# Optimization experiments

Hardware: AMD Instinct MI355X
Metric: run time of the kernel (lower is better)

Reference implementation:

```python
import jax, jax.numpy as jnp
import numpy as np

DIM = 4096
N_HEADS = 32
HEAD_DIM = DIM // N_HEADS
BSZ = 4
SEQLEN = 512
MAX_SEQ = 2048
NEG = -1e9


def _qlinear(x, q, s):
    # int-quantized weight [out,in] dequantized with per-output-channel scale
    w = q.astype(jnp.float32) * s[:, None]
    return jnp.einsum('bsd,od->bso', x, w)


def _apply_rotary(xq, xk, cos, sin):
    # xq,xk: [b,s,h,hd]; cos,sin: [s,hd/2]
    def rot(t):
        b, s, h, d = t.shape
        t = t.reshape(b, s, h, d // 2, 2)
        tr, ti = t[..., 0], t[..., 1]
        c = cos[None, :, None, :]
        sn = sin[None, :, None, :]
        out_r = tr * c - ti * sn
        out_i = tr * sn + ti * c
        return jnp.stack([out_r, out_i], axis=-1).reshape(b, s, h, d)
    return rot(xq), rot(xk)


def setup_inputs() -> dict:
    key = jax.random.key(0)
    ks = jax.random.split(key, 12)
    x = jax.random.normal(ks[0], (BSZ, SEQLEN, DIM), dtype=jnp.float32)
    inv = 1.0 / (10000.0 ** (jnp.arange(0, HEAD_DIM, 2, dtype=jnp.float32) / HEAD_DIM))
    ang = jnp.arange(SEQLEN, dtype=jnp.float32)[:, None] * inv[None, :]
    freqs_cos, freqs_sin = jnp.cos(ang), jnp.sin(ang)
    input_idexes = jnp.arange(SEQLEN, dtype=jnp.int32)  # cache slots being written
    # causal additive mask over full cache: query at position i may attend j <= i
    j = jnp.arange(MAX_SEQ)
    mask = jnp.where(j[None, :] <= input_idexes[:, None], 0.0, NEG).astype(jnp.float32)
    mask = mask[None, None]  # [1,1,S,MAX_SEQ]
    cache_k = jnp.zeros((BSZ, MAX_SEQ, N_HEADS, HEAD_DIM), jnp.float32)
    cache_v = jnp.zeros((BSZ, MAX_SEQ, N_HEADS, HEAD_DIM), jnp.float32)
    SCALE = 2.0 / (127.0 * np.sqrt(DIM))
    def mkw(kq, kscale):
        q = jax.random.randint(kq, (DIM, DIM), -127, 128, dtype=jnp.int32)
        s = jax.random.uniform(kscale, (DIM,), dtype=jnp.float32) * SCALE
        return q, s
    wq_q, wq_s = mkw(ks[1], ks[2])
    wk_q, wk_s = mkw(ks[3], ks[4])
    wv_q, wv_s = mkw(ks[5], ks[6])
    wo_q, wo_s = mkw(ks[7], ks[8])
    return dict(x=x, freqs_cos=freqs_cos, freqs_sin=freqs_sin, mask=mask,
                input_idexes=input_idexes, cache_k=cache_k, cache_v=cache_v,
                wq_q=wq_q, wq_s=wq_s, wk_q=wk_q, wk_s=wk_s,
                wv_q=wv_q, wv_s=wv_s, wo_q=wo_q, wo_s=wo_s)


def reference(x, freqs_cos, freqs_sin, mask, input_idexes, cache_k, cache_v,
              wq_q, wq_s, wk_q, wk_s, wv_q, wv_s, wo_q, wo_s):
    bsz, seqlen, _ = x.shape
    xq = _qlinear(x, wq_q, wq_s).reshape(bsz, seqlen, N_HEADS, HEAD_DIM)
    xk = _qlinear(x, wk_q, wk_s).reshape(bsz, seqlen, N_HEADS, HEAD_DIM)
    xv = _qlinear(x, wv_q, wv_s).reshape(bsz, seqlen, N_HEADS, HEAD_DIM)
    xq, xk = _apply_rotary(xq, xk, freqs_cos, freqs_sin)
    # KV-cache append (index_copy on dim 1)
    cache_k = cache_k.at[:, input_idexes].set(xk)
    cache_v = cache_v.at[:, input_idexes].set(xv)
    # [b,h,q,d] x [b,h,k,d] -> [b,h,q,k]
    scores = jnp.einsum('bqhd,bkhd->bhqk', xq, cache_k) / np.sqrt(HEAD_DIM)
    scores = scores + mask
    probs = jax.nn.softmax(scores.astype(jnp.float32), axis=-1).astype(xq.dtype)
    out = jnp.einsum('bhqk,bkhd->bqhd', probs, cache_v).reshape(bsz, seqlen, -1)
    out = _qlinear(out, wo_q, wo_s)
    return out, (cache_k, cache_v)
```

## Files before the change

kernel.cpp:

```cpp
#include <hip/hip_runtime.h>
#include <cstdint>
#include <cstddef>

typedef __bf16 bf16;
typedef __attribute__((ext_vector_type(8))) __bf16 bf16x8;
typedef __attribute__((ext_vector_type(2))) __bf16 bf16x2;
typedef __attribute__((ext_vector_type(4))) float f32x4;
typedef __attribute__((ext_vector_type(2))) float f32x2;
typedef __attribute__((ext_vector_type(4))) int i32x4;

#define DIMN 4096
#define SEQ 512
#define MAXSEQ 2048
#define NHEAD 32
#define HD 128
#define NBH 128
#define MTOK 2048

#define BM 128
#define BN 128
#define BK 32
#define BKI 64

__device__ __forceinline__ void gld_lds16(const void* g, void* l) {
  __builtin_amdgcn_global_load_lds(
      (const __attribute__((address_space(1))) unsigned int*)g,
      (__attribute__((address_space(3))) unsigned int*)l, 16, 0, 0);
}

__device__ __forceinline__ void gemm_core(const bf16* Ablk, const bf16* Bblk,
                                          int lda, int ldb, int kmax,
                                          f32x4 acc[4][4], bf16* As, bf16* Bs) {
  const int tid = threadIdx.x;
  const int wave = tid >> 6;
  const int lane = tid & 63;
  const int wm = (wave >> 1) * 64;
  const int wn = (wave & 1) * 64;
  const int lrow = lane & 15;
  const int lkq8 = (lane >> 4) * 8;
  const int srow = wave * 32 + (lane >> 2);
  const int scol = (lane & 3) * 8;
  const bf16* Ag = Ablk + (size_t)srow * lda + scol;
  const bf16* Bg = Bblk + (size_t)srow * ldb + scol;
  bf16* lA = As + wave * 32 * BK;
  bf16* lB = Bs + wave * 32 * BK;

  for (int k0 = 0; k0 < kmax; k0 += BK) {
    __syncthreads();
    gld_lds16(Ag + k0, lA);
    gld_lds16(Ag + k0 + (size_t)16 * lda, lA + 16 * BK);
    gld_lds16(Bg + k0, lB);
    gld_lds16(Bg + k0 + (size_t)16 * ldb, lB + 16 * BK);
    __syncthreads();
    bf16x8 a[4], b[4];
#pragma unroll
    for (int i = 0; i < 4; ++i)
      a[i] = *(const bf16x8*)(As + (wm + i * 16 + lrow) * BK + lkq8);
#pragma unroll
    for (int i = 0; i < 4; ++i)
      b[i] = *(const bf16x8*)(Bs + (wn + i * 16 + lrow) * BK + lkq8);
#pragma unroll
    for (int mi = 0; mi < 4; ++mi)
#pragma unroll
      for (int ni = 0; ni < 4; ++ni)
        acc[mi][ni] = __builtin_amdgcn_mfma_f32_16x16x32_bf16(a[mi], b[ni], acc[mi][ni], 0, 0, 0);
  }
}

__device__ __forceinline__ void gemm_core_i8(const char* Ablk, const char* Bblk,
                                             int lda, int ldb, int kmax,
                                             i32x4 acc[4][4], char* As, char* Bs) {
  const int tid = threadIdx.x;
  const int wave = tid >> 6;
  const int lane = tid & 63;
  const int wm = (wave >> 1) * 64;
  const int wn = (wave & 1) * 64;
  const int lrow = lane & 15;
  const int lkq16 = (lane >> 4) * 16;
  const int srow = wave * 32 + (lane >> 2);
  const int scol = (lane & 3) * 16;
  const char* Ag = Ablk + (size_t)srow * lda + scol;
  const char* Bg = Bblk + (size_t)srow * ldb + scol;
  char* lA = As + wave * 32 * BKI;
  char* lB = Bs + wave * 32 * BKI;

  for (int k0 = 0; k0 < kmax; k0 += BKI) {
    __syncthreads();
    gld_lds16(Ag + k0, lA);
    gld_lds16(Ag + k0 + (size_t)16 * lda, lA + 16 * BKI);
    gld_lds16(Bg + k0, lB);
    gld_lds16(Bg + k0 + (size_t)16 * ldb, lB + 16 * BKI);
    __syncthreads();
    i32x4 a[4], b[4];
#pragma unroll
    for (int i = 0; i < 4; ++i)
      a[i] = *(const i32x4*)(As + (wm + i * 16 + lrow) * BKI + lkq16);
#pragma unroll
    for (int i = 0; i < 4; ++i)
      b[i] = *(const i32x4*)(Bs + (wn + i * 16 + lrow) * BKI + lkq16);
#pragma unroll
    for (int mi = 0; mi < 4; ++mi)
#pragma unroll
      for (int ni = 0; ni < 4; ++ni)
        acc[mi][ni] = __builtin_amdgcn_mfma_i32_16x16x64_i8(a[mi], b[ni], acc[mi][ni], 0, 0, 0);
  }
}

#define ACC_INIT_F(acc)                                 \
  f32x4 acc[4][4];                                      \
  _Pragma("unroll") for (int _i = 0; _i < 4; ++_i)      \
      _Pragma("unroll") for (int _j = 0; _j < 4; ++_j)  \
          acc[_i][_j] = f32x4{0.f, 0.f, 0.f, 0.f};

#define ACC_INIT_I(acc)                                 \
  i32x4 acc[4][4];                                      \
  _Pragma("unroll") for (int _i = 0; _i < 4; ++_i)      \
      _Pragma("unroll") for (int _j = 0; _j < 4; ++_j)  \
          acc[_i][_j] = i32x4{0, 0, 0, 0};

#define EPI_COORDS                                      \
  const int lane = threadIdx.x & 63;                    \
  const int wave = threadIdx.x >> 6;                    \
  const int wm = (wave >> 1) * 64, wn = (wave & 1) * 64;\
  const int cq = (lane >> 4) * 4, cc = lane & 15;

__global__ __launch_bounds__(256) void k_cvt_w8(
    const int* __restrict__ q0, const int* __restrict__ q1,
    const int* __restrict__ q2, const int* __restrict__ q3,
    char* __restrict__ w8) {
  const int* q = (blockIdx.y == 0) ? q0 : (blockIdx.y == 1) ? q1
               : (blockIdx.y == 2) ? q2 : q3;
  char* w = w8 + (size_t)blockIdx.y * 16777216ull;
  size_t i = ((size_t)blockIdx.x * 256 + threadIdx.x) * 16;
  const i32x4* qp = (const i32x4*)(q + i);
  i32x4 a = qp[0], b = qp[1], c = qp[2], d = qp[3];
  i32x4 o;
  o[0] = (a[0] & 255) | ((a[1] & 255) << 8) | ((a[2] & 255) << 16) | (a[3] << 24);
  o[1] = (b[0] & 255) | ((b[1] & 255) << 8) | ((b[2] & 255) << 16) | (b[3] << 24);
  o[2] = (c[0] & 255) | ((c[1] & 255) << 8) | ((c[2] & 255) << 16) | (c[3] << 24);
  o[3] = (d[0] & 255) | ((d[1] & 255) << 8) | ((d[2] & 255) << 16) | (d[3] << 24);
  *(i32x4*)(w + i) = o;
}

__global__ __launch_bounds__(256) void k_quant_x(const float* __restrict__ x,
                                                 char* __restrict__ x8,
                                                 float* __restrict__ xs) {
  __shared__ float red[4];
  const int row = blockIdx.x, tid = threadIdx.x;
  const float* src = x + (size_t)row * DIMN + tid * 16;
  f32x4 v[4];
#pragma unroll
  for (int j = 0; j < 4; ++j) v[j] = ((const f32x4*)src)[j];
  float am = 0.f;
#pragma unroll
  for (int j = 0; j < 4; ++j)
#pragma unroll
    for (int e = 0; e < 4; ++e) am = fmaxf(am, fabsf(v[j][e]));
#pragma unroll
  for (int off = 32; off; off >>= 1) am = fmaxf(am, __shfl_xor(am, off, 64));
  if ((tid & 63) == 0) red[tid >> 6] = am;
  __syncthreads();
  am = fmaxf(fmaxf(red[0], red[1]), fmaxf(red[2], red[3]));
  const float inv = am > 0.f ? 127.f / am : 0.f;
  i32x4 o;
#pragma unroll
  for (int j = 0; j < 4; ++j) {
    int b0 = (int)rintf(v[j][0] * inv), b1 = (int)rintf(v[j][1] * inv);
    int b2 = (int)rintf(v[j][2] * inv), b3 = (int)rintf(v[j][3] * inv);
    o[j] = (b0 & 255) | ((b1 & 255) << 8) | ((b2 & 255) << 16) | (b3 << 24);
  }
  *(i32x4*)(x8 + (size_t)row * DIMN + tid * 16) = o;
  if (tid == 0) xs[row] = am * (1.f / 127.f);
}

__global__ __launch_bounds__(256) void k_quant_attn(const bf16* __restrict__ at,
                                                    char* __restrict__ a8,
                                                    float* __restrict__ as_) {
  __shared__ float red[4];
  const int row = blockIdx.x, tid = threadIdx.x;
  const bf16* src = at + (size_t)row * DIMN + tid * 16;
  bf16x8 h0 = ((const bf16x8*)src)[0], h1 = ((const bf16x8*)src)[1];
  float f[16];
#pragma unroll
  for (int j = 0; j < 8; ++j) { f[j] = (float)h0[j]; f[8 + j] = (float)h1[j]; }
  float am = 0.f;
#pragma unroll
  for (int j = 0; j < 16; ++j) am = fmaxf(am, fabsf(f[j]));
#pragma unroll
  for (int off = 32; off; off >>= 1) am = fmaxf(am, __shfl_xor(am, off, 64));
  if ((tid & 63) == 0) red[tid >> 6] = am;
  __syncthreads();
  am = fmaxf(fmaxf(red[0], red[1]), fmaxf(red[2], red[3]));
  const float inv = am > 0.f ? 127.f / am : 0.f;
  i32x4 o;
#pragma unroll
  for (int j = 0; j < 4; ++j) {
    int b0 = (int)rintf(f[j * 4 + 0] * inv), b1 = (int)rintf(f[j * 4 + 1] * inv);
    int b2 = (int)rintf(f[j * 4 + 2] * inv), b3 = (int)rintf(f[j * 4 + 3] * inv);
    o[j] = (b0 & 255) | ((b1 & 255) << 8) | ((b2 & 255) << 16) | (b3 << 24);
  }
  *(i32x4*)(a8 + (size_t)row * DIMN + tid * 16) = o;
  if (tid == 0) as_[row] = am * (1.f / 127.f);
}

__global__ __launch_bounds__(256, 2) void k_gemm_qkv8(
    const char* __restrict__ X8, const char* __restrict__ W8,
    const float* __restrict__ xs, const float* __restrict__ sq,
    const float* __restrict__ sk, const float* __restrict__ sv,
    const float* __restrict__ fc, const float* __restrict__ fs,
    const int* __restrict__ idx, bf16* __restrict__ qbf,
    bf16* __restrict__ kbf, float* __restrict__ ck, float* __restrict__ cv) {
  __shared__ __align__(16) char As[BM * BKI];
  __shared__ __align__(16) char Bs[BN * BKI];
  const int n0 = blockIdx.x * BN;
  const int m0 = blockIdx.y * BM;
  const int z = blockIdx.z;
  const char* W = W8 + (size_t)z * 16777216ull;
  const float* sw = (z == 0) ? sq : (z == 1) ? sk : sv;
  ACC_INIT_I(acc);
  gemm_core_i8(X8 + (size_t)m0 * DIMN, W + (size_t)n0 * DIMN, DIMN, DIMN, DIMN, acc, As, Bs);
  EPI_COORDS;
  if (z < 2) {
    bf16* dst = (z == 0) ? qbf : kbf;
#pragma unroll
    for (int mi = 0; mi < 4; ++mi)
#pragma unroll
      for (int ni = 0; ni < 4; ++ni)
#pragma unroll
        for (int r = 0; r < 4; ++r) {
          const int row = m0 + wm + mi * 16 + cq + r;
          const int col = n0 + wn + ni * 16 + cc;
          const float v = (float)acc[mi][ni][r] * xs[row] * sw[col];
          const float pv = __shfl_xor(v, 1, 64);
          const int s = row & 511, b = row >> 9;
          const int hd = col & 127, h = col >> 7;
          const int d2 = hd >> 1;
          const float c = fc[s * 64 + d2], sn = fs[s * 64 + d2];
          const float o = (col & 1) ? (pv * sn + v * c) : (v * c - pv * sn);
          dst[(((size_t)(b * NHEAD + h)) * SEQ + s) * HD + hd] = (bf16)o;
          if (z == 1) {
            const int pos = idx[s];
            ck[((size_t)b * MAXSEQ + pos) * DIMN + col] = o;
          }
        }
  } else {
#pragma unroll
    for (int mi = 0; mi < 4; ++mi)
#pragma unroll
      for (int ni = 0; ni < 4; ++ni)
#pragma unroll
        for (int r = 0; r < 4; ++r) {
          const int row = m0 + wm + mi * 16 + cq + r;
          const int col = n0 + wn + ni * 16 + cc;
          const int s = row & 511, b = row >> 9;
          cv[((size_t)b * MAXSEQ + s) * DIMN + col] =
              (float)acc[mi][ni][r] * xs[row] * sw[col];
        }
  }
}

__global__ __launch_bounds__(256) void k_vt(const float* __restrict__ cv,
                                            bf16* __restrict__ vt) {
  __shared__ float tile[32][129];
  const int s0 = blockIdx.x * 32;
  const int bh = blockIdx.y;
  const int b = bh >> 5, h = bh & 31;
  const int tid = threadIdx.x;
  const float* src = cv + (size_t)b * MAXSEQ * DIMN + h * HD;
#pragma unroll
  for (int p = 0; p < 16; ++p) {
    const int row = p * 2 + (tid >> 7);
    const int d = tid & 127;
    tile[row][d] = src[(size_t)(s0 + row) * DIMN + d];
  }
  __syncthreads();
  bf16* dst = vt + (size_t)bh * HD * SEQ;
#pragma unroll
  for (int c = 0; c < 16; ++c) {
    const int d = c * 8 + (tid >> 5);
    const int sl = tid & 31;
    dst[(size_t)d * SEQ + s0 + sl] = (bf16)tile[sl][d];
  }
}

__global__ __launch_bounds__(256, 2) void k_gemm_qk(
    const bf16* __restrict__ qb, const bf16* __restrict__ kb,
    bf16* __restrict__ sc) {
  const int n0 = blockIdx.x * BN;
  const int m0 = blockIdx.y * BM;
  if (n0 >= m0 + BM) return;
  const int bh = blockIdx.z;
  __shared__ __align__(16) bf16 As[BM * BK];
  __shared__ __align__(16) bf16 Bs[BN * BK];
  ACC_INIT_F(acc);
  gemm_core(qb + (size_t)bh * SEQ * HD + (size_t)m0 * HD,
            kb + (size_t)bh * SEQ * HD + (size_t)n0 * HD, HD, HD, HD, acc, As, Bs);
  EPI_COORDS;
  bf16* dst = sc + (size_t)bh * SEQ * SEQ;
#pragma unroll
  for (int mi = 0; mi < 4; ++mi)
#pragma unroll
    for (int ni = 0; ni < 4; ++ni)
#pragma unroll
      for (int r = 0; r < 4; ++r) {
        const int row = m0 + wm + mi * 16 + cq + r;
        const int col = n0 + wn + ni * 16 + cc;
        dst[(size_t)row * SEQ + col] = (bf16)(acc[mi][ni][r] * 0.08838834764831845f);
      }
}

__global__ __launch_bounds__(256) void k_softmax(bf16* __restrict__ sc) {
  const int row = blockIdx.x * 4 + (threadIdx.x >> 6);
  const int lane = threadIdx.x & 63;
  const int q = row & 511;
  bf16* p = sc + (size_t)row * SEQ + lane * 8;
  bf16x8 v8 = *(const bf16x8*)p;
  float lv[8];
  float m = -3.0e38f;
#pragma unroll
  for (int j = 0; j < 8; ++j) {
    const int kj = lane * 8 + j;
    lv[j] = (kj <= q) ? (float)v8[j] : -3.0e38f;
    m = fmaxf(m, lv[j]);
  }
#pragma unroll
  for (int off = 32; off; off >>= 1) m = fmaxf(m, __shfl_xor(m, off, 64));
  float e[8];
  float sum = 0.f;
#pragma unroll
  for (int j = 0; j < 8; ++j) {
    e[j] = (lane * 8 + j <= q) ? __expf(lv[j] - m) : 0.f;
    sum += e[j];
  }
#pragma unroll
  for (int off = 32; off; off >>= 1) sum += __shfl_xor(sum, off, 64);
  const float r = 1.f / sum;
  bf16x8 o;
#pragma unroll
  for (int j = 0; j < 8; ++j) o[j] = (bf16)(e[j] * r);
  *(bf16x8*)p = o;
}

__global__ __launch_bounds__(256, 2) void k_gemm_pv(
    const bf16* __restrict__ P, const bf16* __restrict__ vt,
    bf16* __restrict__ attn) {
  const int m0 = blockIdx.y * BM;
  const int bh = blockIdx.z;
  const int kmax = m0 + BM;
  __shared__ __align__(16) bf16 As[BM * BK];
  __shared__ __align__(16) bf16 Bs[BN * BK];
  ACC_INIT_F(acc);
  gemm_core(P + (size_t)bh * SEQ * SEQ + (size_t)m0 * SEQ,
            vt + (size_t)bh * HD * SEQ, SEQ, SEQ, kmax, acc, As, Bs);
  EPI_COORDS;
  const int b = bh >> 5, h = bh & 31;
#pragma unroll
  for (int mi = 0; mi < 4; ++mi)
#pragma unroll
    for (int ni = 0; ni < 4; ++ni)
#pragma unroll
      for (int r = 0; r < 4; ++r) {
        const int row = m0 + wm + mi * 16 + cq + r;
        const int col = wn + ni * 16 + cc;
        attn[((size_t)(b * SEQ + row)) * DIMN + h * HD + col] = (bf16)acc[mi][ni][r];
      }
}

__global__ __launch_bounds__(256, 2) void k_gemm_out8(
    const char* __restrict__ A8, const char* __restrict__ WO8,
    const float* __restrict__ as_, const float* __restrict__ so,
    float* __restrict__ out) {
  __shared__ __align__(16) char As[BM * BKI];
  __shared__ __align__(16) char Bs[BN * BKI];
  const int n0 = blockIdx.x * BN;
  const int m0 = blockIdx.y * BM;
  ACC_INIT_I(acc);
  gemm_core_i8(A8 + (size_t)m0 * DIMN, WO8 + (size_t)n0 * DIMN, DIMN, DIMN, DIMN, acc, As, Bs);
  EPI_COORDS;
#pragma unroll
  for (int mi = 0; mi < 4; ++mi)
#pragma unroll
    for (int ni = 0; ni < 4; ++ni)
#pragma unroll
      for (int r = 0; r < 4; ++r) {
        const int row = m0 + wm + mi * 16 + cq + r;
        const int col = n0 + wn + ni * 16 + cc;
        out[(size_t)row * DIMN + col] = (float)acc[mi][ni][r] * as_[row] * so[col];
      }
}

extern "C" void kernel_launch(void* const* d_in, const int* in_sizes, int n_in,
                              void* d_out, int out_size, void* d_ws, size_t ws_size,
                              hipStream_t stream) {
  const float* x = (const float*)d_in[0];
  const float* fc = (const float*)d_in[1];
  const float* fs = (const float*)d_in[2];
  const int* idx = (const int*)d_in[4];
  const int* wq_q = (const int*)d_in[7];  const float* wq_s = (const float*)d_in[8];
  const int* wk_q = (const int*)d_in[9];  const float* wk_s = (const float*)d_in[10];
  const int* wv_q = (const int*)d_in[11]; const float* wv_s = (const float*)d_in[12];
  const int* wo_q = (const int*)d_in[13]; const float* wo_s = (const float*)d_in[14];

  float* out = (float*)d_out;
  float* ck_out = out + 8388608;
  float* cv_out = ck_out + 33554432;

  char* ws = (char*)d_ws;
  char* W8   = ws;
  char* X8   = ws + 67108864ull;
  float* XS  = (float*)(ws + 75497472ull);
  float* AS  = (float*)(ws + 75513856ull);
  bf16* QBF  = (bf16*)(ws + 83886080ull);
  bf16* KBF  = (bf16*)(ws + 100663296ull);
  bf16* VTB  = (bf16*)(ws + 117440512ull);
  bf16* ATTN = (bf16*)(ws + 134217728ull);
  char* A8   = ws + 150994944ull;
  bf16* SC   = (bf16*)(ws + 167772160ull);

  for (int b = 0; b < 4; ++b) {
    hipMemsetAsync(ck_out + ((size_t)b * MAXSEQ + SEQ) * DIMN, 0, 25165824ull, stream);
    hipMemsetAsync(cv_out + ((size_t)b * MAXSEQ + SEQ) * DIMN, 0, 25165824ull, stream);
  }
  k_cvt_w8<<<dim3(4096, 4), 256, 0, stream>>>(wq_q, wk_q, wv_q, wo_q, W8);
  k_quant_x<<<dim3(2048), 256, 0, stream>>>(x, X8, XS);
  k_gemm_qkv8<<<dim3(32, 16, 3), 256, 0, stream>>>(
      X8, W8, XS, wq_s, wk_s, wv_s, fc, fs, idx, QBF, KBF, ck_out, cv_out);
  k_vt<<<dim3(16, 128), 256, 0, stream>>>(cv_out, VTB);
  k_gemm_qk<<<dim3(4, 4, 128), 256, 0, stream>>>(QBF, KBF, SC);
  k_softmax<<<dim3(16384), 256, 0, stream>>>(SC);
  k_gemm_pv<<<dim3(1, 4, 128), 256, 0, stream>>>(SC, VTB, ATTN);
  k_quant_attn<<<dim3(2048), 256, 0, stream>>>(ATTN, A8, AS);
  k_gemm_out8<<<dim3(32, 16), 256, 0, stream>>>(A8, W8 + 50331648ull, AS, wo_s, out);
  (void)in_sizes; (void)n_in; (void)out_size; (void)ws_size;
}
```

Measured before the change: 902.3 us.

## Widen int8 GEMM K-tile with swizzled LDS, fuse prep launches, compact causal QK grid

The int8 GEMM core now stages 128-wide K slices instead of 64, using an XOR-swizzled LDS layout that is meant to avoid bank conflicts on fragment reads and to halve the number of barriers per K. Weight conversion, activation quantization and the zeroing of the KV-cache tails are merged into a single prep kernel, replacing two launches plus eight memset calls. The QK score GEMM launches only the 10 lower-triangular tiles via a constant lookup table instead of launching 16 and returning early from 6. The larger LDS footprint per block may reduce occupancy.

```diff
diff --git a/kernel.cpp b/kernel.cpp
--- a/kernel.cpp
+++ b/kernel.cpp
@@ -20,7 +20,7 @@
 #define BM 128
 #define BN 128
 #define BK 32
-#define BKI 64
+#define BKI 128
 
 __device__ __forceinline__ void gld_lds16(const void* g, void* l) {
   __builtin_amdgcn_global_load_lds(
@@ -76,9 +76,9 @@
   const int wm = (wave >> 1) * 64;
   const int wn = (wave & 1) * 64;
   const int lrow = lane & 15;
-  const int lkq16 = (lane >> 4) * 16;
-  const int srow = wave * 32 + (lane >> 2);
-  const int scol = (lane & 3) * 16;
+  const int q = lane >> 4;
+  const int srow = wave * 32 + (lane >> 3);
+  const int scol = (((lane & 7) ^ ((lane >> 3) & 7)) * 16);
   const char* Ag = Ablk + (size_t)srow * lda + scol;
   const char* Bg = Bblk + (size_t)srow * ldb + scol;
   char* lA = As + wave * 32 * BKI;
@@ -86,23 +86,33 @@
 
   for (int k0 = 0; k0 < kmax; k0 += BKI) {
     __syncthreads();
-    gld_lds16(Ag + k0, lA);
-    gld_lds16(Ag + k0 + (size_t)16 * lda, lA + 16 * BKI);
-    gld_lds16(Bg + k0, lB);
-    gld_lds16(Bg + k0 + (size_t)16 * ldb, lB + 16 * BKI);
+#pragma unroll
+    for (int r = 0; r < 4; ++r) {
+      gld_lds16(Ag + k0 + (size_t)(8 * r) * lda, lA + 8 * r * BKI);
+      gld_lds16(Bg + k0 + (size_t)(8 * r) * ldb, lB + 8 * r * BKI);
+    }
     __syncthreads();
-    i32x4 a[4], b[4];
-#pragma unroll
-    for (int i = 0; i < 4; ++i)
-      a[i] = *(const i32x4*)(As + (wm + i * 16 + lrow) * BKI + lkq16);
-#pragma unroll
-    for (int i = 0; i < 4; ++i)
-      b[i] = *(const i32x4*)(Bs + (wn + i * 16 + lrow) * BKI + lkq16);
-#pragma unroll
-    for (int mi = 0; mi < 4; ++mi)
-#pragma unroll
-      for (int ni = 0; ni < 4; ++ni)
-        acc[mi][ni] = __builtin_amdgcn_mfma_i32_16x16x64_i8(a[mi], b[ni], acc[mi][ni], 0, 0, 0);
+#pragma unroll
+    for (int kk = 0; kk < 2; ++kk) {
+      i32x4 a[4], b[4];
+#pragma unroll
+      for (int i = 0; i < 4; ++i) {
+        const int row = wm + i * 16 + lrow;
+        const int slot = (kk * 4 + q) ^ (lrow & 7);
+        a[i] = *(const i32x4*)(As + row * BKI + slot * 16);
+      }
+#pragma unroll
+      for (int i = 0; i < 4; ++i) {
+        const int row = wn + i * 16 + lrow;
+        const int slot = (kk * 4 + q) ^ (lrow & 7);
+        b[i] = *(const i32x4*)(Bs + row * BKI + slot * 16);
+      }
+#pragma unroll
+      for (int mi = 0; mi < 4; ++mi)
+#pragma unroll
+        for (int ni = 0; ni < 4; ++ni)
+          acc[mi][ni] = __builtin_amdgcn_mfma_i32_16x16x64_i8(a[mi], b[ni], acc[mi][ni], 0, 0, 0);
+    }
   }
 }
 
@@ -124,53 +134,63 @@
   const int wm = (wave >> 1) * 64, wn = (wave & 1) * 64;\
   const int cq = (lane >> 4) * 4, cc = lane & 15;
 
-__global__ __launch_bounds__(256) void k_cvt_w8(
+__global__ __launch_bounds__(256) void k_prep(
     const int* __restrict__ q0, const int* __restrict__ q1,
     const int* __restrict__ q2, const int* __restrict__ q3,
-    char* __restrict__ w8) {
-  const int* q = (blockIdx.y == 0) ? q0 : (blockIdx.y == 1) ? q1
-               : (blockIdx.y == 2) ? q2 : q3;
-  char* w = w8 + (size_t)blockIdx.y * 16777216ull;
-  size_t i = ((size_t)blockIdx.x * 256 + threadIdx.x) * 16;
-  const i32x4* qp = (const i32x4*)(q + i);
-  i32x4 a = qp[0], b = qp[1], c = qp[2], d = qp[3];
-  i32x4 o;
-  o[0] = (a[0] & 255) | ((a[1] & 255) << 8) | ((a[2] & 255) << 16) | (a[3] << 24);
-  o[1] = (b[0] & 255) | ((b[1] & 255) << 8) | ((b[2] & 255) << 16) | (b[3] << 24);
-  o[2] = (c[0] & 255) | ((c[1] & 255) << 8) | ((c[2] & 255) << 16) | (c[3] << 24);
-  o[3] = (d[0] & 255) | ((d[1] & 255) << 8) | ((d[2] & 255) << 16) | (d[3] << 24);
-  *(i32x4*)(w + i) = o;
-}
-
-__global__ __launch_bounds__(256) void k_quant_x(const float* __restrict__ x,
-                                                 char* __restrict__ x8,
-                                                 float* __restrict__ xs) {
+    char* __restrict__ w8, const float* __restrict__ x,
+    char* __restrict__ x8, float* __restrict__ xs,
+    float* __restrict__ ck, float* __restrict__ cv) {
   __shared__ float red[4];
-  const int row = blockIdx.x, tid = threadIdx.x;
-  const float* src = x + (size_t)row * DIMN + tid * 16;
-  f32x4 v[4];
-#pragma unroll
-  for (int j = 0; j < 4; ++j) v[j] = ((const f32x4*)src)[j];
-  float am = 0.f;
-#pragma unroll
-  for (int j = 0; j < 4; ++j)
-#pragma unroll
-    for (int e = 0; e < 4; ++e) am = fmaxf(am, fabsf(v[j][e]));
-#pragma unroll
-  for (int off = 32; off; off >>= 1) am = fmaxf(am, __shfl_xor(am, off, 64));
-  if ((tid & 63) == 0) red[tid >> 6] = am;
-  __syncthreads();
-  am = fmaxf(fmaxf(red[0], red[1]), fmaxf(red[2], red[3]));
-  const float inv = am > 0.f ? 127.f / am : 0.f;
-  i32x4 o;
-#pragma unroll
-  for (int j = 0; j < 4; ++j) {
-    int b0 = (int)rintf(v[j][0] * inv), b1 = (int)rintf(v[j][1] * inv);
-    int b2 = (int)rintf(v[j][2] * inv), b3 = (int)rintf(v[j][3] * inv);
-    o[j] = (b0 & 255) | ((b1 & 255) << 8) | ((b2 & 255) << 16) | (b3 << 24);
-  }
-  *(i32x4*)(x8 + (size_t)row * DIMN + tid * 16) = o;
-  if (tid == 0) xs[row] = am * (1.f / 127.f);
+  const int bx = blockIdx.x;
+  const int tid = threadIdx.x;
+  if (bx < 16384) {
+    const int w = bx >> 12;
+    const int* q = (w == 0) ? q0 : (w == 1) ? q1 : (w == 2) ? q2 : q3;
+    char* wp = w8 + (size_t)w * 16777216ull;
+    size_t i = ((size_t)(bx & 4095) * 256 + tid) * 16;
+    const i32x4* qp = (const i32x4*)(q + i);
+    i32x4 a = qp[0], b = qp[1], c = qp[2], d = qp[3];
+    i32x4 o;
+    o[0] = (a[0] & 255) | ((a[1] & 255) << 8) | ((a[2] & 255) << 16) | (a[3] << 24);
+    o[1] = (b[0] & 255) | ((b[1] & 255) << 8) | ((b[2] & 255) << 16) | (b[3] << 24);
+    o[2] = (c[0] & 255) | ((c[1] & 255) << 8) | ((c[2] & 255) << 16) | (c[3] << 24);
+    o[3] = (d[0] & 255) | ((d[1] & 255) << 8) | ((d[2] & 255) << 16) | (d[3] << 24);
+    *(i32x4*)(wp + i) = o;
+  } else if (bx < 18432) {
+    const int row = bx - 16384;
+    const float* src = x + (size_t)row * DIMN + tid * 16;
+    f32x4 v[4];
+#pragma unroll
+    for (int j = 0; j < 4; ++j) v[j] = ((const f32x4*)src)[j];
+    float am = 0.f;
+#pragma unroll
+    for (int j = 0; j < 4; ++j)
+#pragma unroll
+      for (int e = 0; e < 4; ++e) am = fmaxf(am, fabsf(v[j][e]));
+#pragma unroll
+    for (int off = 32; off; off >>= 1) am = fmaxf(am, __shfl_xor(am, off, 64));
+    if ((tid & 63) == 0) red[tid >> 6] = am;
+    __syncthreads();
+    am = fmaxf(fmaxf(red[0], red[1]), fmaxf(red[2], red[3]));
+    const float inv = am > 0.f ? 127.f / am : 0.f;
+    i32x4 o;
+#pragma unroll
+    for (int j = 0; j < 4; ++j) {
+      int b0 = (int)rintf(v[j][0] * inv), b1 = (int)rintf(v[j][1] * inv);
+      int b2 = (int)rintf(v[j][2] * inv), b3 = (int)rintf(v[j][3] * inv);
+      o[j] = (b0 & 255) | ((b1 & 255) << 8) | ((b2 & 255) << 16) | (b3 << 24);
+    }
+    *(i32x4*)(x8 + (size_t)row * DIMN + tid * 16) = o;
+    if (tid == 0) xs[row] = am * (1.f / 127.f);
+  } else {
+    const int z = bx - 18432;
+    const int region = z / 6144;
+    const int zoff = z - region * 6144;
+    const int b = region >> 1;
+    float* base = (region & 1) ? cv : ck;
+    char* p = (char*)(base + ((size_t)b * MAXSEQ + SEQ) * DIMN);
+    *(f32x4*)(p + (size_t)zoff * 4096 + tid * 16) = f32x4{0.f, 0.f, 0.f, 0.f};
+  }
 }
 
 __global__ __launch_bounds__(256) void k_quant_attn(const bf16* __restrict__ at,
@@ -283,12 +303,14 @@
   }
 }
 
+__constant__ int g_tm[10] = {0, 1, 1, 2, 2, 2, 3, 3, 3, 3};
+__constant__ int g_tn[10] = {0, 0, 1, 0, 1, 2, 0, 1, 2, 3};
+
 __global__ __launch_bounds__(256, 2) void k_gemm_qk(
     const bf16* __restrict__ qb, const bf16* __restrict__ kb,
     bf16* __restrict__ sc) {
-  const int n0 = blockIdx.x * BN;
-  const int m0 = blockIdx.y * BM;
-  if (n0 >= m0 + BM) return;
+  const int m0 = g_tm[blockIdx.x] * BM;
+  const int n0 = g_tn[blockIdx.x] * BN;
   const int bh = blockIdx.z;
   __shared__ __align__(16) bf16 As[BM * BK];
   __shared__ __align__(16) bf16 Bs[BN * BK];
@@ -396,10 +418,14 @@
   const float* fc = (const float*)d_in[1];
   const float* fs = (const float*)d_in[2];
   const int* idx = (const int*)d_in[4];
-  const int* wq_q = (const int*)d_in[7];  const float* wq_s = (const float*)d_in[8];
-  const int* wk_q = (const int*)d_in[9];  const float* wk_s = (const float*)d_in[10];
-  const int* wv_q = (const int*)d_in[11]; const float* wv_s = (const float*)d_in[12];
-  const int* wo_q = (const int*)d_in[13]; const float* wo_s = (const float*)d_in[14];
+  const int* wq_q = (const int*)d_in[7];
+  const int* wk_q = (const int*)d_in[9];
+  const int* wv_q = (const int*)d_in[11];
+  const int* wo_q = (const int*)d_in[13];
+  const float* wq_s = (const float*)d_in[8];
+  const float* wk_s = (const float*)d_in[10];
+  const float* wv_s = (const float*)d_in[12];
+  const float* wo_s = (const float*)d_in[14];
 
   float* out = (float*)d_out;
   float* ck_out = out + 8388608;
@@ -417,16 +443,12 @@
   char* A8   = ws + 150994944ull;
   bf16* SC   = (bf16*)(ws + 167772160ull);
 
-  for (int b = 0; b < 4; ++b) {
-    hipMemsetAsync(ck_out + ((size_t)b * MAXSEQ + SEQ) * DIMN, 0, 25165824ull, stream);
-    hipMemsetAsync(cv_out + ((size_t)b * MAXSEQ + SEQ) * DIMN, 0, 25165824ull, stream);
-  }
-  k_cvt_w8<<<dim3(4096, 4), 256, 0, stream>>>(wq_q, wk_q, wv_q, wo_q, W8);
-  k_quant_x<<<dim3(2048), 256, 0, stream>>>(x, X8, XS);
+  k_prep<<<dim3(67584), 256, 0, stream>>>(wq_q, wk_q, wv_q, wo_q, W8, x, X8, XS,
+                                          ck_out, cv_out);
   k_gemm_qkv8<<<dim3(32, 16, 3), 256, 0, stream>>>(
       X8, W8, XS, wq_s, wk_s, wv_s, fc, fs, idx, QBF, KBF, ck_out, cv_out);
   k_vt<<<dim3(16, 128), 256, 0, stream>>>(cv_out, VTB);
-  k_gemm_qk<<<dim3(4, 4, 128), 256, 0, stream>>>(QBF, KBF, SC);
+  k_gemm_qk<<<dim3(10, 1, 128), 256, 0, stream>>>(QBF, KBF, SC);
   k_softmax<<<dim3(16384), 256, 0, stream>>>(SC);
   k_gemm_pv<<<dim3(1, 4, 128), 256, 0, stream>>>(SC, VTB, ATTN);
   k_quant_attn<<<dim3(2048), 256, 0, stream>>>(ATTN, A8, AS);
```

Result: faster. 873.7 us (-3.2%).
